# Optimization experiments

Measured on AMD Instinct MI355X. Metric: run time of the kernel, lower is better.

Reference implementation:

```python
import jax, jax.numpy as jnp
import numpy as np

C = 1024
GROUPS = 32
EPS = 1e-5
K = 20


def group_norm(v, weight, bias):
    # v: [B, C]; normalize per group of C//GROUPS channels (torch GroupNorm on 2D input)
    B = v.shape[0]
    g = v.reshape(B, GROUPS, C // GROUPS)
    mean = g.mean(axis=-1, keepdims=True)
    var = g.var(axis=-1, keepdims=True)
    g = (g - mean) * jax.lax.rsqrt(var + EPS)
    return g.reshape(B, C) * weight + bias


def setup_inputs() -> dict:
    key = jax.random.key(0)
    ks = jax.random.split(key, 16)
    B, L = 32, 2048
    s = 1.0 / np.sqrt(C)
    inp = {
        "x": jax.random.normal(ks[0], (B, L, C), dtype=jnp.float32),
        "W": jax.random.uniform(ks[1], (C, C), jnp.float32, -s, s),
        "b": jax.random.uniform(ks[2], (C,), jnp.float32, -s, s),
        "W1": jax.random.uniform(ks[3], (C, C), jnp.float32, -s, s),
        "b1": jax.random.uniform(ks[4], (C,), jnp.float32, -s, s),
        "Wm": jax.random.uniform(ks[5], (C, C), jnp.float32, -s, s),
        "bm": jax.random.uniform(ks[6], (C,), jnp.float32, -s, s),
        "Wa": jax.random.uniform(ks[7], (C, C), jnp.float32, -s, s),
        "ba": jax.random.uniform(ks[8], (C,), jnp.float32, -s, s),
        "g1_w": jnp.ones((C,), jnp.float32),
        "g1_b": jnp.zeros((C,), jnp.float32),
        "g2_w": jnp.ones((C,), jnp.float32),
        "g2_b": jnp.zeros((C,), jnp.float32),
    }
    return inp


def reference(x, W, b, W1, b1, Wm, bm, Wa, ba, g1_w, g1_b, g2_w, g2_b):
    # x: [B, L, C]
    x = jnp.einsum('blc,dc->bld', x, W) + b          # self.linear
    x_M = x.mean(axis=1)                              # adaptive avg pool over L -> [B, C]
    x_M = group_norm(x_M @ Wm.T + bm, g1_w, g1_b)     # linear_max + gn1
    x_A = x.max(axis=1)                               # adaptive max pool over L -> [B, C]
    x_A = group_norm(x_A @ Wa.T + ba, g2_w, g2_b)     # linear_Aug + gn2
    x = jnp.einsum('blc,dc->bld', x, W1) + b1         # self.linear1
    out1 = jnp.einsum('blc,bc->bl', x, x_M)           # x @ x_M^T, squeezed
    out2 = jnp.einsum('blc,bc->bl', x, x_A)
    out = jax.nn.softmax(out1, axis=1) * jax.nn.softmax(out2, axis=1)  # [B, L]
    _, topk_idx = jax.lax.top_k(out, K)               # [B, K]
    selected = jnp.take_along_axis(x, topk_idx[:, :, None], axis=1)  # [B, K, C]
    return selected
```

## Files before the change

### kernel.cpp

```cpp
#include <hip/hip_runtime.h>

#define L_SEQ 2048
#define CH    1024
#define NB    32
#define KSEL  20

typedef short v8s  __attribute__((ext_vector_type(8)));
typedef float v16f __attribute__((ext_vector_type(16)));

#define WS_XSUM   0
#define WS_YMAX   32768
#define WS_M1     65536
#define WS_AMAX   98304
#define WS_T1     131072
#define WS_T2     163840
#define WS_P      196608
#define WS_V      294912
#define WS_S      327680
#define WS_TOPK   393216
#define WS_BC     394240
#define WS_WC     395264
#define WS_WPAK   1443840
#define WS_WTPAK  2492416

__device__ __forceinline__ void split8(float4 qa, float4 qb, uint4& hi, uint4& lo) {
  float f[8] = {qa.x, qa.y, qa.z, qa.w, qb.x, qb.y, qb.z, qb.w};
  unsigned h[8], l[8];
  #pragma unroll
  for (int e = 0; e < 8; ++e) {
    unsigned u  = __float_as_uint(f[e]);
    unsigned hu = u & 0xFFFF0000u;
    float lf    = f[e] - __uint_as_float(hu);
    h[e] = u >> 16;
    l[e] = __float_as_uint(lf) >> 16;
  }
  hi.x = h[0] | (h[1] << 16); hi.y = h[2] | (h[3] << 16);
  hi.z = h[4] | (h[5] << 16); hi.w = h[6] | (h[7] << 16);
  lo.x = l[0] | (l[1] << 16); lo.y = l[2] | (l[3] << 16);
  lo.z = l[4] | (l[5] << 16); lo.w = l[6] | (l[7] << 16);
}

__global__ __launch_bounds__(256) void packw_kernel(const float* __restrict__ W,
                                                    uint4* __restrict__ wp,
                                                    float* __restrict__ zws) {
  int t = threadIdx.x, kt = blockIdx.x, Rw = blockIdx.y;
  if (zws) {
    int flat = (Rw * 32 + kt) * 256 + t;
    zws[WS_XSUM + flat] = 0.f;
    if (flat < 32768) zws[WS_V + flat] = 0.f;
  }
  const float* wb = W + (size_t)Rw * 128 * CH;
  uint4* out = wp + ((size_t)Rw * 32 + kt) * 1024;
  #pragma unroll
  for (int pass = 0; pass < 2; ++pass) {
    int idx = pass * 256 + t;
    int r = idx >> 2, p = idx & 3;
    const float* ap = wb + (size_t)r * CH + kt * 32 + p * 8;
    float4 f0 = *(const float4*)ap;
    float4 f1 = *(const float4*)(ap + 4);
    uint4 hi, lo;
    split8(f0, f1, hi, lo);
    int slot = ((r >> 5) * 2 + (p >> 1)) * 128 + (p & 1) * 32 + (r & 31);
    out[slot] = hi;
    out[slot + 64] = lo;
  }
}

__global__ __launch_bounds__(256) void packwt_kernel(const float* __restrict__ W,
                                                     uint4* __restrict__ wtp) {
  __shared__ float Wl[32][129];
  int t = threadIdx.x, kt = blockIdx.x, cc = blockIdx.y;
  #pragma unroll
  for (int it = 0; it < 16; ++it) {
    int idx = it * 256 + t;
    int el = idx >> 7, cl = idx & 127;
    Wl[el][cl] = W[(size_t)(kt * 32 + el) * CH + cc * 128 + cl];
  }
  __syncthreads();
  uint4* out = wtp + ((size_t)cc * 32 + kt) * 1024;
  #pragma unroll
  for (int pass = 0; pass < 2; ++pass) {
    int sid = pass * 256 + t;
    int r = sid >> 2, p = sid & 3;
    float f[8];
    #pragma unroll
    for (int q = 0; q < 8; ++q) f[q] = Wl[p * 8 + q][r];
    float4 f0 = {f[0], f[1], f[2], f[3]}, f1 = {f[4], f[5], f[6], f[7]};
    uint4 hi, lo;
    split8(f0, f1, hi, lo);
    int slot = ((r >> 5) * 2 + (p >> 1)) * 128 + (p & 1) * 32 + (r & 31);
    out[slot] = hi;
    out[slot + 64] = lo;
  }
}

__global__ __launch_bounds__(256) void mean_kernel(const float* __restrict__ x,
                                                   float* __restrict__ xsum) {
  int b = blockIdx.y, chunk = blockIdx.x, t = threadIdx.x;
  const float4* bp = (const float4*)(x + ((size_t)b * L_SEQ + (size_t)chunk * 64) * CH);
  float sx = 0.f, sy = 0.f, sz = 0.f, sw = 0.f;
  #pragma unroll 4
  for (int l = 0; l < 64; ++l) {
    float4 a = bp[l * 256 + t];
    sx += a.x; sy += a.y; sz += a.z; sw += a.w;
  }
  float* dst = xsum + b * CH + t * 4;
  atomicAdd(dst + 0, sx); atomicAdd(dst + 1, sy);
  atomicAdd(dst + 2, sz); atomicAdd(dst + 3, sw);
}

template<bool FOURTH>
__device__ __forceinline__ void gemm_core(const float* __restrict__ arow,
                                          const uint4* __restrict__ wbB,
                                          const int cgbase,
                                          uint4 (*__restrict__ smA)[1024],
                                          const int w, const int lane,
                                          v16f acc[4][2]) {
  {
    float4 p0 = *(const float4*)(arow);
    float4 p1 = *(const float4*)(arow + 4);
    float4 p2 = *(const float4*)(arow + 16);
    float4 p3 = *(const float4*)(arow + 20);
    uint4 hi, lo;
    split8(p0, p1, hi, lo);
    smA[0][(w * 2 + 0) * 128 + lane] = hi;
    smA[0][(w * 2 + 0) * 128 + 64 + lane] = lo;
    split8(p2, p3, hi, lo);
    smA[0][(w * 2 + 1) * 128 + lane] = hi;
    smA[0][(w * 2 + 1) * 128 + 64 + lane] = lo;
  }
  v8s bc[4], bn[4];
  #pragma unroll
  for (int j = 0; j < 2; ++j) {
    bc[j * 2]     = *(const v8s*)&wbB[((cgbase + j) * 2 + 0) * 128];
    bc[j * 2 + 1] = *(const v8s*)&wbB[((cgbase + j) * 2 + 0) * 128 + 64];
  }
  __syncthreads();

  for (int kt = 0; kt < 32; ++kt) {
    const int cur = kt & 1;
    float4 q0, q1, q2, q3;
    if (kt < 31) {
      const float* an = arow + (kt + 1) * 32;
      q0 = *(const float4*)(an);
      q1 = *(const float4*)(an + 4);
      q2 = *(const float4*)(an + 16);
      q3 = *(const float4*)(an + 20);
    }
    #pragma unroll
    for (int s = 0; s < 2; ++s) {
      const int nkt = s ? kt + 1 : kt, ns = s ^ 1;
      if (nkt < 32) {
        #pragma unroll
        for (int j = 0; j < 2; ++j) {
          bn[j * 2]     = *(const v8s*)&wbB[(size_t)nkt * 1024 + ((cgbase + j) * 2 + ns) * 128];
          bn[j * 2 + 1] = *(const v8s*)&wbB[(size_t)nkt * 1024 + ((cgbase + j) * 2 + ns) * 128 + 64];
        }
      }
      v8s ah[4], al[4];
      #pragma unroll
      for (int i = 0; i < 4; ++i) {
        int base = (i * 2 + s) * 128 + lane;
        ah[i] = *(const v8s*)&smA[cur][base];
        al[i] = *(const v8s*)&smA[cur][base + 64];
      }
      #pragma unroll
      for (int j = 0; j < 2; ++j) {
        v8s bh = bc[j * 2], bl = bc[j * 2 + 1];
        #pragma unroll
        for (int i = 0; i < 4; ++i) {
          acc[i][j] = __builtin_amdgcn_mfma_f32_32x32x16_bf16(ah[i], bh, acc[i][j], 0, 0, 0);
          acc[i][j] = __builtin_amdgcn_mfma_f32_32x32x16_bf16(ah[i], bl, acc[i][j], 0, 0, 0);
          acc[i][j] = __builtin_amdgcn_mfma_f32_32x32x16_bf16(al[i], bh, acc[i][j], 0, 0, 0);
          if (FOURTH)
            acc[i][j] = __builtin_amdgcn_mfma_f32_32x32x16_bf16(al[i], bl, acc[i][j], 0, 0, 0);
        }
      }
      #pragma unroll
      for (int e = 0; e < 4; ++e) bc[e] = bn[e];
    }
    if (kt < 31) {
      uint4 hi, lo;
      split8(q0, q1, hi, lo);
      smA[cur ^ 1][(w * 2 + 0) * 128 + lane] = hi;
      smA[cur ^ 1][(w * 2 + 0) * 128 + 64 + lane] = lo;
      split8(q2, q3, hi, lo);
      smA[cur ^ 1][(w * 2 + 1) * 128 + lane] = hi;
      smA[cur ^ 1][(w * 2 + 1) * 128 + 64 + lane] = lo;
    }
    __syncthreads();
  }
}

__global__ __launch_bounds__(256, 2) void gemm_max5(const float* __restrict__ X,
                                                    const uint4* __restrict__ wp,
                                                    unsigned* __restrict__ ymax) {
  __shared__ uint4 smA[2][1024];
  const int t = threadIdx.x, lane = t & 63, w = t >> 6;
  const int blk = blockIdx.x;
  const int strip = blk & 3, mt = blk >> 2;
  const int batch = mt >> 4;
  const float* arow = X + (size_t)(mt * 128 + w * 32 + (lane & 31)) * CH + (lane >> 5) * 8;
  v16f acc[4][2];
  #pragma unroll
  for (int i = 0; i < 4; ++i)
    #pragma unroll
    for (int j = 0; j < 2; ++j)
      #pragma unroll
      for (int e = 0; e < 16; ++e) acc[i][j][e] = 0.f;
  const uint4* wbB = wp + (size_t)(strip * 2 + (w >> 1)) * 32768 + lane;
  gemm_core<false>(arow, wbB, (w & 1) * 2, smA, w, lane, acc);

  #pragma unroll
  for (int j = 0; j < 2; ++j) {
    float m = -INFINITY;
    #pragma unroll
    for (int i = 0; i < 4; ++i)
      #pragma unroll
      for (int e = 0; e < 16; ++e) m = fmaxf(m, acc[i][j][e]);
    m = fmaxf(m, __shfl_xor(m, 32));
    if (lane < 32) {
      int col = strip * 256 + w * 64 + j * 32 + lane;
      unsigned u = __float_as_uint(m);
      unsigned enc = (m >= 0.f) ? (u | 0x80000000u) : ~u;
      atomicMax(&ymax[batch * CH + col], enc);
    }
  }
}

__global__ __launch_bounds__(256, 2) void wc_gemm(const float* __restrict__ W1,
                                                  const uint4* __restrict__ wtp,
                                                  float* __restrict__ Wc) {
  __shared__ uint4 smA[2][1024];
  const int t = threadIdx.x, lane = t & 63, w = t >> 6;
  const int blk = blockIdx.x;
  const int strip = blk & 3, mt = blk >> 2;
  const float* arow = W1 + (size_t)(mt * 128 + w * 32 + (lane & 31)) * CH + (lane >> 5) * 8;
  v16f acc[4][2];
  #pragma unroll
  for (int i = 0; i < 4; ++i)
    #pragma unroll
    for (int j = 0; j < 2; ++j)
      #pragma unroll
      for (int e = 0; e < 16; ++e) acc[i][j][e] = 0.f;
  const uint4* wbB = wtp + (size_t)(strip * 2 + (w >> 1)) * 32768 + lane;
  gemm_core<true>(arow, wbB, (w & 1) * 2, smA, w, lane, acc);

  #pragma unroll
  for (int i = 0; i < 4; ++i)
    #pragma unroll
    for (int j = 0; j < 2; ++j)
      #pragma unroll
      for (int r = 0; r < 16; ++r) {
        int row = (r & 3) + 8 * (r >> 2) + 4 * (lane >> 5);
        int grow = mt * 128 + i * 32 + row;
        int gcol = strip * 256 + w * 64 + j * 32 + (lane & 31);
        Wc[(size_t)grow * CH + gcol] = acc[i][j][r];
      }
}

__global__ __launch_bounds__(256, 2) void out_gemm(const float* __restrict__ X,
                                                   const int* __restrict__ idx,
                                                   const uint4* __restrict__ wcp,
                                                   const float* __restrict__ bc,
                                                   float* __restrict__ C) {
  __shared__ uint4 smA[2][1024];
  const int t = threadIdx.x, lane = t & 63, w = t >> 6;
  const int blk = blockIdx.x;
  const int strip = blk & 3, mt = blk >> 2;
  const int rr = mt * 128 + w * 32 + (lane & 31);
  const int grow_a = (rr / KSEL) * L_SEQ + idx[rr];
  const float* arow = X + (size_t)grow_a * CH + (lane >> 5) * 8;
  v16f acc[4][2];
  #pragma unroll
  for (int i = 0; i < 4; ++i)
    #pragma unroll
    for (int j = 0; j < 2; ++j)
      #pragma unroll
      for (int e = 0; e < 16; ++e) acc[i][j][e] = 0.f;
  const uint4* wbB = wcp + (size_t)(strip * 2 + (w >> 1)) * 32768 + lane;
  gemm_core<true>(arow, wbB, (w & 1) * 2, smA, w, lane, acc);

  #pragma unroll
  for (int i = 0; i < 4; ++i)
    #pragma unroll
    for (int j = 0; j < 2; ++j)
      #pragma unroll
      for (int r = 0; r < 16; ++r) {
        int row = (r & 3) + 8 * (r >> 2) + 4 * (lane >> 5);
        int grow = mt * 128 + i * 32 + row;
        int gcol = strip * 256 + w * 64 + j * 32 + (lane & 31);
        C[(size_t)grow * CH + gcol] = acc[i][j][r] + bc[gcol];
      }
}

__global__ __launch_bounds__(256) void bc_kernel(const float* __restrict__ W1,
                                                 const float* __restrict__ b,
                                                 const float* __restrict__ b1,
                                                 float* __restrict__ bc) {
  int t = threadIdx.x;
  int d = blockIdx.x * 8 + (t >> 5);
  int lane = t & 31;
  const float4* wr = (const float4*)(W1 + (size_t)d * CH);
  const float4* br = (const float4*)b;
  float acc = 0.f;
  #pragma unroll
  for (int c = lane; c < 256; c += 32) {
    float4 a = wr[c], m = br[c];
    acc += a.x * m.x + a.y * m.y + a.z * m.z + a.w * m.w;
  }
  #pragma unroll
  for (int off = 16; off; off >>= 1) acc += __shfl_xor(acc, off);
  if (lane == 0) bc[d] = acc + b1[d];
}

__global__ __launch_bounds__(256) void poolmix_kernel(const float* __restrict__ xsum,
                                                      const unsigned* __restrict__ ymax,
                                                      const float* __restrict__ W,
                                                      const float* __restrict__ bias,
                                                      float* __restrict__ m1,
                                                      float* __restrict__ amax) {
  int t = threadIdx.x;
  int id = blockIdx.x * 256 + t;
  unsigned u = ymax[id];
  float f = (u & 0x80000000u) ? __uint_as_float(u & 0x7FFFFFFFu) : __uint_as_float(~u);
  amax[id] = f + bias[id & (CH - 1)];

  int d = blockIdx.x * 8 + (t >> 5);
  int b = t & 31;
  const float4* Ir = (const float4*)(xsum + b * CH);
  const float4* Mr = (const float4*)(W + (size_t)d * CH);
  float acc = 0.f;
  #pragma unroll 4
  for (int c = 0; c < CH / 4; ++c) {
    float4 a = Ir[c], m = Mr[c];
    acc += a.x * m.x + a.y * m.y + a.z * m.z + a.w * m.w;
  }
  m1[b * CH + d] = acc * (1.f / 2048.f) + bias[d];
}

__global__ __launch_bounds__(256) void lin2_kernel(const float* __restrict__ m1,
                                                   const float* __restrict__ amax,
                                                   const float* __restrict__ Wm,
                                                   const float* __restrict__ bm,
                                                   const float* __restrict__ Wa,
                                                   const float* __restrict__ ba,
                                                   float* __restrict__ t1,
                                                   float* __restrict__ t2) {
  int t = threadIdx.x;
  int which = blockIdx.x >> 7, bk = blockIdx.x & 127;
  const float* I = which ? amax : m1;
  const float* M = which ? Wa : Wm;
  const float* bb = which ? ba : bm;
  float* O = which ? t2 : t1;
  int d = bk * 8 + (t >> 5);
  int b = t & 31;
  const float4* Ir = (const float4*)(I + b * CH);
  const float4* Mr = (const float4*)(M + (size_t)d * CH);
  float acc = 0.f;
  #pragma unroll 4
  for (int c = 0; c < CH / 4; ++c) {
    float4 a = Ir[c], m = Mr[c];
    acc += a.x * m.x + a.y * m.y + a.z * m.z + a.w * m.w;
  }
  O[b * CH + d] = acc + bb[d];
}

__global__ __launch_bounds__(1024) void gnp_kernel(const float* __restrict__ t1,
                                                   const float* __restrict__ t2,
                                                   const float* __restrict__ g1w, const float* __restrict__ g1b,
                                                   const float* __restrict__ g2w, const float* __restrict__ g2b,
                                                   float* __restrict__ p) {
  int b = blockIdx.x, c = threadIdx.x;
  float v1 = t1[b * CH + c], v2 = t2[b * CH + c];
  float s1 = v1, s2 = v2;
  #pragma unroll
  for (int off = 16; off; off >>= 1) { s1 += __shfl_xor(s1, off); s2 += __shfl_xor(s2, off); }
  float d1 = v1 - s1 * (1.f / 32.f), d2 = v2 - s2 * (1.f / 32.f);
  float q1 = d1 * d1, q2 = d2 * d2;
  #pragma unroll
  for (int off = 16; off; off >>= 1) { q1 += __shfl_xor(q1, off); q2 += __shfl_xor(q2, off); }
  float o1 = d1 * rsqrtf(q1 * (1.f / 32.f) + 1e-5f) * g1w[c] + g1b[c];
  float o2 = d2 * rsqrtf(q2 * (1.f / 32.f) + 1e-5f) * g2w[c] + g2b[c];
  p[b * CH + c] = o1 + o2;
}

__global__ __launch_bounds__(256) void colmm_kernel(const float* __restrict__ S,
                                                    const float* __restrict__ M,
                                                    float* __restrict__ O) {
  __shared__ float Sl[128][32];
  int t = threadIdx.x;
  int e0 = (blockIdx.x & 3) * 256, c0 = (blockIdx.x >> 2) * 128;
  for (int i = t; i < 4096; i += 256) {
    int c = i >> 5, b = i & 31;
    Sl[c][b] = S[b * CH + c0 + c];
  }
  __syncthreads();
  int e = e0 + t;
  float acc[32];
  #pragma unroll
  for (int b = 0; b < 32; ++b) acc[b] = 0.f;
  for (int c = 0; c < 128; ++c) {
    float wv = M[(size_t)(c0 + c) * CH + e];
    #pragma unroll
    for (int b = 0; b < 32; ++b) acc[b] += Sl[c][b] * wv;
  }
  #pragma unroll
  for (int b = 0; b < 32; ++b) atomicAdd(&O[b * CH + e], acc[b]);
}

__global__ __launch_bounds__(256) void logits_kernel(const float* __restrict__ x,
                                                     const float* __restrict__ v,
                                                     float* __restrict__ s) {
  __shared__ float4 vl[256];
  int b = blockIdx.y, chunk = blockIdx.x, t = threadIdx.x;
  vl[t] = ((const float4*)(v + b * CH))[t];
  __syncthreads();
  int wv = t >> 6, lane = t & 63;
  for (int it = 0; it < 8; ++it) {
    int l = chunk * 32 + it * 4 + wv;
    const float4* xr = (const float4*)(x + ((size_t)b * L_SEQ + l) * CH);
    float acc = 0.f;
    #pragma unroll
    for (int rep = 0; rep < 4; ++rep) {
      float4 a = xr[rep * 64 + lane];
      float4 c = vl[rep * 64 + lane];
      acc += a.x * c.x + a.y * c.y + a.z * c.z + a.w * c.w;
    }
    #pragma unroll
    for (int off = 32; off; off >>= 1) acc += __shfl_xor(acc, off);
    if (lane == 0) s[b * L_SEQ + l] = acc;
  }
}

__global__ __launch_bounds__(256) void topk_kernel(const float* __restrict__ s,
                                                   int* __restrict__ idx_out) {
  int b = blockIdx.x, t = threadIdx.x;
  int lane = t & 63, w = t >> 6;
  __shared__ float lv[4];
  __shared__ int   li[4];
  float v[8];
  #pragma unroll
  for (int j = 0; j < 8; ++j) v[j] = s[b * L_SEQ + j * 256 + t];
  for (int k = 0; k < KSEL; ++k) {
    float bv = -INFINITY; int bi = 1 << 30;
    #pragma unroll
    for (int j = 0; j < 8; ++j) {
      int gi = j * 256 + t;
      if (v[j] > bv || (v[j] == bv && gi < bi)) { bv = v[j]; bi = gi; }
    }
    #pragma unroll
    for (int off = 32; off; off >>= 1) {
      float ov = __shfl_xor(bv, off); int oi = __shfl_xor(bi, off);
      if (ov > bv || (ov == bv && oi < bi)) { bv = ov; bi = oi; }
    }
    if (lane == 0) { lv[w] = bv; li[w] = bi; }
    __syncthreads();
    float fv = lv[0]; int fi = li[0];
    #pragma unroll
    for (int w2 = 1; w2 < 4; ++w2) {
      float ov = lv[w2]; int oi = li[w2];
      if (ov > fv || (ov == fv && oi < fi)) { fv = ov; fi = oi; }
    }
    if (t == 0) idx_out[b * KSEL + k] = fi;
    if ((fi & 255) == t) v[fi >> 8] = -INFINITY;
    __syncthreads();
  }
}

extern "C" void kernel_launch(void* const* d_in, const int* in_sizes, int n_in,
                              void* d_out, int out_size, void* d_ws, size_t ws_size,
                              hipStream_t stream) {
  const float* x   = (const float*)d_in[0];
  const float* W   = (const float*)d_in[1];
  const float* b   = (const float*)d_in[2];
  const float* W1  = (const float*)d_in[3];
  const float* b1  = (const float*)d_in[4];
  const float* Wm  = (const float*)d_in[5];
  const float* bm  = (const float*)d_in[6];
  const float* Wa  = (const float*)d_in[7];
  const float* ba  = (const float*)d_in[8];
  const float* g1w = (const float*)d_in[9];
  const float* g1b = (const float*)d_in[10];
  const float* g2w = (const float*)d_in[11];
  const float* g2b = (const float*)d_in[12];

  float* wsf = (float*)d_ws;
  float*    xsum = wsf + WS_XSUM;
  unsigned* ymax = (unsigned*)(wsf + WS_YMAX);
  float*    m1   = wsf + WS_M1;
  float*    amax = wsf + WS_AMAX;
  float*    t1   = wsf + WS_T1;
  float*    t2   = wsf + WS_T2;
  float*    p    = wsf + WS_P;
  float*    vvec = wsf + WS_V;
  float*    sbuf = wsf + WS_S;
  int*      tidx = (int*)(wsf + WS_TOPK);
  float*    bcv  = wsf + WS_BC;
  float*    Wc   = wsf + WS_WC;
  uint4*    wpak = (uint4*)(wsf + WS_WPAK);
  uint4*    wtpak = (uint4*)(wsf + WS_WTPAK);

  packw_kernel<<<dim3(32, 8), 256, 0, stream>>>(W, wpak, wsf);
  packwt_kernel<<<dim3(32, 8), 256, 0, stream>>>(W, wtpak);
  mean_kernel<<<dim3(32, 32), 256, 0, stream>>>(x, xsum);
  gemm_max5<<<2048, 256, 0, stream>>>(x, wpak, ymax);

  wc_gemm<<<32, 256, 0, stream>>>(W1, wtpak, Wc);
  bc_kernel<<<128, 256, 0, stream>>>(W1, b, b1, bcv);
  packw_kernel<<<dim3(32, 8), 256, 0, stream>>>(Wc, wtpak, nullptr);

  poolmix_kernel<<<128, 256, 0, stream>>>(xsum, ymax, W, b, m1, amax);
  lin2_kernel<<<256, 256, 0, stream>>>(m1, amax, Wm, bm, Wa, ba, t1, t2);
  gnp_kernel<<<32, 1024, 0, stream>>>(t1, t2, g1w, g1b, g2w, g2b, p);
  colmm_kernel<<<32, 256, 0, stream>>>(p, Wc, vvec);
  logits_kernel<<<dim3(64, 32), 256, 0, stream>>>(x, vvec, sbuf);
  topk_kernel<<<32, 256, 0, stream>>>(sbuf, tidx);
  out_gemm<<<20, 256, 0, stream>>>(x, tidx, wtpak, bcv, (float*)d_out);
}
```

Measured before the change: 1.047 ms.

## Split-K the small GEMMs with atomics and fuse prep kernels into one launch

wc_gemm and out_gemm launched only 32 and 20 blocks. They now split the K dimension across 4 and 8 chunks and accumulate into zero-initialised outputs with atomicAdd, which fills more CUs. The packing, workspace zeroing, Wc zeroing and bias precompute are merged into a single prep_kernel, cutting launch count. The output is pre-filled with the bias inside gnp_kernel before out_gemm adds into it. The trade-off is extra atomic traffic, extra zeroing writes, and summation order that now varies from run to run.

Result: faster. 963.0 us (-8.0%).

```diff
diff --git a/kernel.cpp b/kernel.cpp
--- a/kernel.cpp
+++ b/kernel.cpp
@@ -40,15 +40,9 @@
   lo.z = l[4] | (l[5] << 16); lo.w = l[6] | (l[7] << 16);
 }
 
-__global__ __launch_bounds__(256) void packw_kernel(const float* __restrict__ W,
-                                                    uint4* __restrict__ wp,
-                                                    float* __restrict__ zws) {
-  int t = threadIdx.x, kt = blockIdx.x, Rw = blockIdx.y;
-  if (zws) {
-    int flat = (Rw * 32 + kt) * 256 + t;
-    zws[WS_XSUM + flat] = 0.f;
-    if (flat < 32768) zws[WS_V + flat] = 0.f;
-  }
+__device__ __forceinline__ void pack_row_body(const float* __restrict__ W,
+                                              uint4* __restrict__ wp,
+                                              int Rw, int kt, int t) {
   const float* wb = W + (size_t)Rw * 128 * CH;
   uint4* out = wp + ((size_t)Rw * 32 + kt) * 1024;
   #pragma unroll
@@ -66,10 +60,10 @@
   }
 }
 
-__global__ __launch_bounds__(256) void packwt_kernel(const float* __restrict__ W,
-                                                     uint4* __restrict__ wtp) {
-  __shared__ float Wl[32][129];
-  int t = threadIdx.x, kt = blockIdx.x, cc = blockIdx.y;
+__device__ __forceinline__ void pack_tr_body(const float* __restrict__ W,
+                                             uint4* __restrict__ wtp,
+                                             int cc, int kt, int t,
+                                             float (*__restrict__ Wl)[129]) {
   #pragma unroll
   for (int it = 0; it < 16; ++it) {
     int idx = it * 256 + t;
@@ -92,6 +86,50 @@
     out[slot] = hi;
     out[slot + 64] = lo;
   }
+}
+
+__global__ __launch_bounds__(256) void prep_kernel(const float* __restrict__ W,
+                                                   const float* __restrict__ W1,
+                                                   const float* __restrict__ b,
+                                                   const float* __restrict__ b1,
+                                                   uint4* __restrict__ wp,
+                                                   uint4* __restrict__ wtp,
+                                                   float* __restrict__ wsf,
+                                                   float* __restrict__ bc) {
+  __shared__ float Wl[32][129];
+  int t = threadIdx.x, x = blockIdx.x, y = blockIdx.y;
+  if (y < 8) {
+    int flat = (y * 32 + x) * 256 + t;
+    wsf[WS_XSUM + flat] = 0.f;
+    if (flat < 32768) wsf[WS_V + flat] = 0.f;
+    pack_row_body(W, wp, y, x, t);
+  } else if (y < 16) {
+    int tid = ((y - 8) * 32 + x) * 256 + t;
+    float4* wc4 = (float4*)(wsf + WS_WC);
+    #pragma unroll
+    for (int r = 0; r < 4; ++r) wc4[(size_t)tid * 4 + r] = float4{0.f, 0.f, 0.f, 0.f};
+    pack_tr_body(W, wtp, y - 8, x, t, Wl);
+  } else {
+    int bk = (y - 16) * 32 + x;
+    int d = bk * 8 + (t >> 5);
+    int lane = t & 31;
+    const float4* wr = (const float4*)(W1 + (size_t)d * CH);
+    const float4* br = (const float4*)b;
+    float acc = 0.f;
+    #pragma unroll
+    for (int c = lane; c < 256; c += 32) {
+      float4 a = wr[c], m = br[c];
+      acc += a.x * m.x + a.y * m.y + a.z * m.z + a.w * m.w;
+    }
+    #pragma unroll
+    for (int off = 16; off; off >>= 1) acc += __shfl_xor(acc, off);
+    if (lane == 0) bc[d] = acc + b1[d];
+  }
+}
+
+__global__ __launch_bounds__(256) void packw_kernel(const float* __restrict__ W,
+                                                    uint4* __restrict__ wp) {
+  pack_row_body(W, wp, blockIdx.y, blockIdx.x, threadIdx.x);
 }
 
 __global__ __launch_bounds__(256) void mean_kernel(const float* __restrict__ x,
@@ -109,7 +147,7 @@
   atomicAdd(dst + 2, sz); atomicAdd(dst + 3, sw);
 }
 
-template<bool FOURTH>
+template<bool FOURTH, int NKT>
 __device__ __forceinline__ void gemm_core(const float* __restrict__ arow,
                                           const uint4* __restrict__ wbB,
                                           const int cgbase,
@@ -137,10 +175,10 @@
   }
   __syncthreads();
 
-  for (int kt = 0; kt < 32; ++kt) {
+  for (int kt = 0; kt < NKT; ++kt) {
     const int cur = kt & 1;
     float4 q0, q1, q2, q3;
-    if (kt < 31) {
+    if (kt < NKT - 1) {
       const float* an = arow + (kt + 1) * 32;
       q0 = *(const float4*)(an);
       q1 = *(const float4*)(an + 4);
@@ -150,7 +188,7 @@
     #pragma unroll
     for (int s = 0; s < 2; ++s) {
       const int nkt = s ? kt + 1 : kt, ns = s ^ 1;
-      if (nkt < 32) {
+      if (nkt < NKT) {
         #pragma unroll
         for (int j = 0; j < 2; ++j) {
           bn[j * 2]     = *(const v8s*)&wbB[(size_t)nkt * 1024 + ((cgbase + j) * 2 + ns) * 128];
@@ -179,7 +217,7 @@
       #pragma unroll
       for (int e = 0; e < 4; ++e) bc[e] = bn[e];
     }
-    if (kt < 31) {
+    if (kt < NKT - 1) {
       uint4 hi, lo;
       split8(q0, q1, hi, lo);
       smA[cur ^ 1][(w * 2 + 0) * 128 + lane] = hi;
@@ -209,7 +247,7 @@
       #pragma unroll
       for (int e = 0; e < 16; ++e) acc[i][j][e] = 0.f;
   const uint4* wbB = wp + (size_t)(strip * 2 + (w >> 1)) * 32768 + lane;
-  gemm_core<false>(arow, wbB, (w & 1) * 2, smA, w, lane, acc);
+  gemm_core<false, 32>(arow, wbB, (w & 1) * 2, smA, w, lane, acc);
 
   #pragma unroll
   for (int j = 0; j < 2; ++j) {
@@ -233,9 +271,10 @@
                                                   float* __restrict__ Wc) {
   __shared__ uint4 smA[2][1024];
   const int t = threadIdx.x, lane = t & 63, w = t >> 6;
-  const int blk = blockIdx.x;
+  const int blk = blockIdx.x, chunk = blockIdx.y;
   const int strip = blk & 3, mt = blk >> 2;
-  const float* arow = W1 + (size_t)(mt * 128 + w * 32 + (lane & 31)) * CH + (lane >> 5) * 8;
+  const float* arow = W1 + (size_t)(mt * 128 + w * 32 + (lane & 31)) * CH
+                         + (lane >> 5) * 8 + chunk * 256;
   v16f acc[4][2];
   #pragma unroll
   for (int i = 0; i < 4; ++i)
@@ -243,8 +282,9 @@
     for (int j = 0; j < 2; ++j)
       #pragma unroll
       for (int e = 0; e < 16; ++e) acc[i][j][e] = 0.f;
-  const uint4* wbB = wtp + (size_t)(strip * 2 + (w >> 1)) * 32768 + lane;
-  gemm_core<true>(arow, wbB, (w & 1) * 2, smA, w, lane, acc);
+  const uint4* wbB = wtp + (size_t)(strip * 2 + (w >> 1)) * 32768
+                         + (size_t)chunk * (8 * 1024) + lane;
+  gemm_core<true, 8>(arow, wbB, (w & 1) * 2, smA, w, lane, acc);
 
   #pragma unroll
   for (int i = 0; i < 4; ++i)
@@ -255,22 +295,21 @@
         int row = (r & 3) + 8 * (r >> 2) + 4 * (lane >> 5);
         int grow = mt * 128 + i * 32 + row;
         int gcol = strip * 256 + w * 64 + j * 32 + (lane & 31);
-        Wc[(size_t)grow * CH + gcol] = acc[i][j][r];
+        atomicAdd(&Wc[(size_t)grow * CH + gcol], acc[i][j][r]);
       }
 }
 
 __global__ __launch_bounds__(256, 2) void out_gemm(const float* __restrict__ X,
                                                    const int* __restrict__ idx,
                                                    const uint4* __restrict__ wcp,
-                                                   const float* __restrict__ bc,
                                                    float* __restrict__ C) {
   __shared__ uint4 smA[2][1024];
   const int t = threadIdx.x, lane = t & 63, w = t >> 6;
-  const int blk = blockIdx.x;
+  const int blk = blockIdx.x, chunk = blockIdx.y;
   const int strip = blk & 3, mt = blk >> 2;
   const int rr = mt * 128 + w * 32 + (lane & 31);
   const int grow_a = (rr / KSEL) * L_SEQ + idx[rr];
-  const float* arow = X + (size_t)grow_a * CH + (lane >> 5) * 8;
+  const float* arow = X + (size_t)grow_a * CH + (lane >> 5) * 8 + chunk * 128;
   v16f acc[4][2];
   #pragma unroll
   for (int i = 0; i < 4; ++i)
@@ -278,8 +317,9 @@
     for (int j = 0; j < 2; ++j)
       #pragma unroll
       for (int e = 0; e < 16; ++e) acc[i][j][e] = 0.f;
-  const uint4* wbB = wcp + (size_t)(strip * 2 + (w >> 1)) * 32768 + lane;
-  gemm_core<true>(arow, wbB, (w & 1) * 2, smA, w, lane, acc);
+  const uint4* wbB = wcp + (size_t)(strip * 2 + (w >> 1)) * 32768
+                         + (size_t)chunk * (4 * 1024) + lane;
+  gemm_core<true, 4>(arow, wbB, (w & 1) * 2, smA, w, lane, acc);
 
   #pragma unroll
   for (int i = 0; i < 4; ++i)
@@ -290,28 +330,8 @@
         int row = (r & 3) + 8 * (r >> 2) + 4 * (lane >> 5);
         int grow = mt * 128 + i * 32 + row;
         int gcol = strip * 256 + w * 64 + j * 32 + (lane & 31);
-        C[(size_t)grow * CH + gcol] = acc[i][j][r] + bc[gcol];
+        atomicAdd(&C[(size_t)grow * CH + gcol], acc[i][j][r]);
       }
-}
-
-__global__ __launch_bounds__(256) void bc_kernel(const float* __restrict__ W1,
-                                                 const float* __restrict__ b,
-                                                 const float* __restrict__ b1,
-                                                 float* __restrict__ bc) {
-  int t = threadIdx.x;
-  int d = blockIdx.x * 8 + (t >> 5);
-  int lane = t & 31;
-  const float4* wr = (const float4*)(W1 + (size_t)d * CH);
-  const float4* br = (const float4*)b;
-  float acc = 0.f;
-  #pragma unroll
-  for (int c = lane; c < 256; c += 32) {
-    float4 a = wr[c], m = br[c];
-    acc += a.x * m.x + a.y * m.y + a.z * m.z + a.w * m.w;
-  }
-  #pragma unroll
-  for (int off = 16; off; off >>= 1) acc += __shfl_xor(acc, off);
-  if (lane == 0) bc[d] = acc + b1[d];
 }
 
 __global__ __launch_bounds__(256) void poolmix_kernel(const float* __restrict__ xsum,
@@ -370,7 +390,9 @@
                                                    const float* __restrict__ t2,
                                                    const float* __restrict__ g1w, const float* __restrict__ g1b,
                                                    const float* __restrict__ g2w, const float* __restrict__ g2b,
-                                                   float* __restrict__ p) {
+                                                   float* __restrict__ p,
+                                                   const float* __restrict__ bc,
+                                                   float* __restrict__ dout) {
   int b = blockIdx.x, c = threadIdx.x;
   float v1 = t1[b * CH + c], v2 = t2[b * CH + c];
   float s1 = v1, s2 = v2;
@@ -383,6 +405,11 @@
   float o1 = d1 * rsqrtf(q1 * (1.f / 32.f) + 1e-5f) * g1w[c] + g1b[c];
   float o2 = d2 * rsqrtf(q2 * (1.f / 32.f) + 1e-5f) * g2w[c] + g2b[c];
   p[b * CH + c] = o1 + o2;
+
+  int g = b * CH + c;
+  float bcc = bc[c];
+  #pragma unroll
+  for (int r = 0; r < KSEL; ++r) dout[(size_t)r * (NB * CH) + g] = bcc;
 }
 
 __global__ __launch_bounds__(256) void colmm_kernel(const float* __restrict__ S,
@@ -501,20 +528,18 @@
   uint4*    wpak = (uint4*)(wsf + WS_WPAK);
   uint4*    wtpak = (uint4*)(wsf + WS_WTPAK);
 
-  packw_kernel<<<dim3(32, 8), 256, 0, stream>>>(W, wpak, wsf);
-  packwt_kernel<<<dim3(32, 8), 256, 0, stream>>>(W, wtpak);
+  prep_kernel<<<dim3(32, 20), 256, 0, stream>>>(W, W1, b, b1, wpak, wtpak, wsf, bcv);
   mean_kernel<<<dim3(32, 32), 256, 0, stream>>>(x, xsum);
   gemm_max5<<<2048, 256, 0, stream>>>(x, wpak, ymax);
 
-  wc_gemm<<<32, 256, 0, stream>>>(W1, wtpak, Wc);
-  bc_kernel<<<128, 256, 0, stream>>>(W1, b, b1, bcv);
-  packw_kernel<<<dim3(32, 8), 256, 0, stream>>>(Wc, wtpak, nullptr);
+  wc_gemm<<<dim3(32, 4), 256, 0, stream>>>(W1, wtpak, Wc);
+  packw_kernel<<<dim3(32, 8), 256, 0, stream>>>(Wc, wtpak);
 
   poolmix_kernel<<<128, 256, 0, stream>>>(xsum, ymax, W, b, m1, amax);
   lin2_kernel<<<256, 256, 0, stream>>>(m1, amax, Wm, bm, Wa, ba, t1, t2);
-  gnp_kernel<<<32, 1024, 0, stream>>>(t1, t2, g1w, g1b, g2w, g2b, p);
+  gnp_kernel<<<32, 1024, 0, stream>>>(t1, t2, g1w, g1b, g2w, g2b, p, bcv, (float*)d_out);
   colmm_kernel<<<32, 256, 0, stream>>>(p, Wc, vvec);
   logits_kernel<<<dim3(64, 32), 256, 0, stream>>>(x, vvec, sbuf);
   topk_kernel<<<32, 256, 0, stream>>>(sbuf, tidx);
-  out_gemm<<<20, 256, 0, stream>>>(x, tidx, wtpak, bcv, (float*)d_out);
-}
+  out_gemm<<<dim3(20, 8), 256, 0, stream>>>(x, tidx, wtpak, (float*)d_out);
+}
```
